# Kernel optimization log

Measured on AMD Instinct MI355X. Metric: run time of the kernel, lower is better.

## Reference

```python
import jax, jax.numpy as jnp
import numpy as np

NUM_HEADS = 8


def setup_inputs() -> dict:
    key0 = jax.random.key(0)
    ks = jax.random.split(key0, 12)
    N, M, B, C = 512, 512, 1, 256
    inp = {
        "query": jax.random.normal(ks[0], (N, B, C), dtype=jnp.float32),
        "key": jax.random.normal(ks[1], (M, B, C), dtype=jnp.float32),
        "value": jax.random.normal(ks[2], (M, B, C), dtype=jnp.float32),
        "embed_g": jax.random.normal(ks[3], (B, N, M, C), dtype=jnp.float32),
        "Wq": jax.random.normal(ks[4], (C, C), dtype=jnp.float32) * 0.02,
        "bq": jnp.zeros((C,), dtype=jnp.float32),
        "Wk": jax.random.normal(ks[5], (C, C), dtype=jnp.float32) * 0.02,
        "bk": jnp.zeros((C,), dtype=jnp.float32),
        "Wv": jax.random.normal(ks[6], (C, C), dtype=jnp.float32) * 0.02,
        "bv": jnp.zeros((C,), dtype=jnp.float32),
        "Wg": jax.random.normal(ks[7], (C, C), dtype=jnp.float32) * 0.02,
        "bg": jnp.zeros((C,), dtype=jnp.float32),
    }
    return inp


def reference(query, key, value, embed_g, Wq, bq, Wk, bk, Wv, bv, Wg, bg):
    H = NUM_HEADS
    N, B, C = query.shape
    M = key.shape[0]
    Dh = C // H

    # torch nn.Linear: x @ W.T + b
    q = (query @ Wq.T + bq).reshape(N, B, H, Dh).transpose(1, 2, 0, 3)   # (B,H,N,Dh)
    k = (key @ Wk.T + bk).reshape(M, B, H, Dh).transpose(1, 2, 0, 3)     # (B,H,M,Dh)
    v = (value @ Wv.T + bv).reshape(M, B, H, Dh).transpose(1, 2, 0, 3)   # (B,H,M,Dh)
    g = (embed_g @ Wg.T + bg).reshape(B, N, M, H, Dh).transpose(0, 3, 1, 2, 4)  # (B,H,N,M,Dh)

    scores_p = jnp.einsum('bhnc,bhnmc->bhnm', q, g)
    scores_e = jnp.einsum('bhnc,bhmc->bhnm', q, k)
    scores = (scores_e + scores_p) / jnp.sqrt(jnp.asarray(Dh, dtype=q.dtype))
    attn = jax.nn.softmax(scores, axis=-1)                               # (B,H,N,M)

    hidden = jnp.einsum('bhnm,bhmd->bhnd', attn, v)                      # (B,H,N,Dh)
    hidden = hidden.transpose(0, 2, 1, 3).reshape(B, N, C)               # (B,N,C)
    hidden = hidden.transpose(1, 0, 2)                                   # (N,B,C)
    return hidden, attn
```

## Files before the change

### kernel.cpp

```cpp
#include <hip/hip_runtime.h>


template <int CTRL, int RMASK>
__device__ __forceinline__ float dpp_add(float v) {
  int x = __builtin_amdgcn_update_dpp(0, __float_as_int(v), CTRL, RMASK, 0xf, false);
  return v + __int_as_float(x);
}

__global__ __launch_bounds__(256) void k_transpose(const float* __restrict__ Wq,
                                                   const float* __restrict__ Wk,
                                                   const float* __restrict__ Wv,
                                                   float* __restrict__ wt) {
  const float* W = (blockIdx.y == 0) ? Wq : (blockIdx.y == 1) ? Wk : Wv;
  float* O = wt + (size_t)blockIdx.y * 65536;
  __shared__ float t[64][65];
  const int tile = blockIdx.x;
  const int tr = (tile >> 2) * 64, tc = (tile & 3) * 64;
  const int c = threadIdx.x & 63, r0 = threadIdx.x >> 6;
#pragma unroll
  for (int i = 0; i < 16; ++i) {
    int r = r0 + i * 4;
    t[r][c] = W[(tr + r) * 256 + tc + c];
  }
  __syncthreads();
#pragma unroll
  for (int i = 0; i < 16; ++i) {
    int r = r0 + i * 4;
    O[(tc + r) * 256 + tr + c] = t[c][r];
  }
}

__global__ __launch_bounds__(256) void k_proj(const float* __restrict__ q_in,
                                              const float* __restrict__ k_in,
                                              const float* __restrict__ v_in,
                                              const float* __restrict__ bq,
                                              const float* __restrict__ bk,
                                              const float* __restrict__ bv,
                                              const float* __restrict__ wt,
                                              float* __restrict__ outb) {
  const int mat = blockIdx.y;
  const float* x = mat == 0 ? q_in : mat == 1 ? k_in : v_in;
  const float* b = mat == 0 ? bq : mat == 1 ? bk : bv;
  const float* WT = wt + (size_t)mat * 65536;
  float* out = outb + (size_t)mat * 131072;

  __shared__ float xl[8][256];
  const int tid = threadIdx.x;
  const int n0 = blockIdx.x * 8;
  for (int idx = tid; idx < 2048; idx += 256)
    xl[idx >> 8][idx & 255] = x[(n0 + (idx >> 8)) * 256 + (idx & 255)];
  __syncthreads();

  float acc[8] = {0.f, 0.f, 0.f, 0.f, 0.f, 0.f, 0.f, 0.f};
  for (int j = 0; j < 256; j += 4) {
    const float w0 = WT[(j + 0) * 256 + tid];
    const float w1 = WT[(j + 1) * 256 + tid];
    const float w2 = WT[(j + 2) * 256 + tid];
    const float w3 = WT[(j + 3) * 256 + tid];
#pragma unroll
    for (int r = 0; r < 8; ++r) {
      const float4 xv = *(const float4*)&xl[r][j];
      acc[r] += xv.x * w0 + xv.y * w1 + xv.z * w2 + xv.w * w3;
    }
  }
  const float bb = b[tid];
#pragma unroll
  for (int r = 0; r < 8; ++r) out[(n0 + r) * 256 + tid] = acc[r] + bb;
}

__global__ __launch_bounds__(256) void k_tfold(const float* __restrict__ qkv,
                                               const float* __restrict__ Wg,
                                               const float* __restrict__ bg,
                                               float* __restrict__ t_ws,
                                               float* __restrict__ qb_ws) {
  const int h = blockIdx.y;
  const int n0 = blockIdx.x * 64;
  const int tid = threadIdx.x;
  const float scale = 0.17677669529663687f;
  __shared__ float wg_s[32][256];
  __shared__ float qs[64][32];
  __shared__ float bgs[32];

  for (int idx = tid; idx < 8192; idx += 256)
    wg_s[idx >> 8][idx & 255] = Wg[(size_t)(h * 32 + (idx >> 8)) * 256 + (idx & 255)];
  for (int idx = tid; idx < 2048; idx += 256)
    qs[idx >> 5][idx & 31] = qkv[(size_t)(n0 + (idx >> 5)) * 256 + h * 32 + (idx & 31)];
  if (tid < 32) bgs[tid] = bg[h * 32 + tid];
  __syncthreads();

  float wr[32];
#pragma unroll
  for (int i = 0; i < 32; ++i) wr[i] = wg_s[i][tid];
  for (int nn = 0; nn < 64; ++nn) {
    float a = 0.f;
#pragma unroll
    for (int i = 0; i < 32; ++i) a = fmaf(qs[nn][i], wr[i], a);
    t_ws[(size_t)(n0 + nn) * 2048 + h * 256 + tid] = a * scale;
  }
  if (tid < 64) {
    float a = 0.f;
#pragma unroll
    for (int i = 0; i < 32; ++i) a = fmaf(qs[tid][i], bgs[i], a);
    qb_ws[(n0 + tid) * 8 + h] = a * scale;
  }
}

__global__ __launch_bounds__(512, 4) void k_main(const float* __restrict__ Eg,
                                                 const float* __restrict__ qkv,
                                                 const float* __restrict__ t_ws,
                                                 const float* __restrict__ qb_ws,
                                                 float* __restrict__ out) {
  const float* k_g = qkv + 131072;
  const float* v_g = qkv + 262144;
  const int n = blockIdx.x;
  const int tid = threadIdx.x;
  const int lane = tid & 63, w = tid >> 6;
  const int s = lane & 31, g = lane >> 5;
  const float scale = 0.17677669529663687f;
  float* attn = out + 131072;

  __shared__ float sc[4096];
  __shared__ float invd[8];
  __shared__ float pv[2][256];

  float t_r[8][8];
#pragma unroll
  for (int h = 0; h < 8; ++h) {
    const float4 a = *(const float4*)(t_ws + (size_t)n * 2048 + h * 256 + s * 8);
    const float4 b = *(const float4*)(t_ws + (size_t)n * 2048 + h * 256 + s * 8 + 4);
    t_r[h][0] = a.x; t_r[h][1] = a.y; t_r[h][2] = a.z; t_r[h][3] = a.w;
    t_r[h][4] = b.x; t_r[h][5] = b.y; t_r[h][6] = b.z; t_r[h][7] = b.w;
  }
  float q_r[8];
  {
    const float4 a = *(const float4*)(qkv + n * 256 + s * 8);
    const float4 b = *(const float4*)(qkv + n * 256 + s * 8 + 4);
    q_r[0] = a.x * scale; q_r[1] = a.y * scale; q_r[2] = a.z * scale; q_r[3] = a.w * scale;
    q_r[4] = b.x * scale; q_r[5] = b.y * scale; q_r[6] = b.z * scale; q_r[7] = b.w * scale;
  }
  float qb_r[8];
#pragma unroll
  for (int h = 0; h < 8; ++h) qb_r[h] = qb_ws[n * 8 + h];
  float msk[8];
#pragma unroll
  for (int h = 0; h < 8; ++h) msk[h] = ((s >> 2) == h) ? 1.f : 0.f;

  const float* E0 = Eg + ((size_t)n * 512 + w * 64 + g) * 256 + s * 8;
  const float* K0 = k_g + (size_t)(w * 64 + g) * 256 + s * 8;
  int m = w * 64 + g;

#pragma unroll 2
  for (int it = 0; it < 32; ++it) {
    const float4 e0 = *(const float4*)(E0);
    const float4 e1 = *(const float4*)(E0 + 4);
    const float4 k0 = *(const float4*)(K0);
    const float4 k1 = *(const float4*)(K0 + 4);
    float kacc;
    kacc = k0.x * q_r[0];             kacc = fmaf(k0.y, q_r[1], kacc);
    kacc = fmaf(k0.z, q_r[2], kacc);  kacc = fmaf(k0.w, q_r[3], kacc);
    kacc = fmaf(k1.x, q_r[4], kacc);  kacc = fmaf(k1.y, q_r[5], kacc);
    kacc = fmaf(k1.z, q_r[6], kacc);  kacc = fmaf(k1.w, q_r[7], kacc);
#pragma unroll
    for (int h = 0; h < 8; ++h) {
      float v = msk[h] * kacc;
      v = fmaf(e0.x, t_r[h][0], v); v = fmaf(e0.y, t_r[h][1], v);
      v = fmaf(e0.z, t_r[h][2], v); v = fmaf(e0.w, t_r[h][3], v);
      v = fmaf(e1.x, t_r[h][4], v); v = fmaf(e1.y, t_r[h][5], v);
      v = fmaf(e1.z, t_r[h][6], v); v = fmaf(e1.w, t_r[h][7], v);
      v = dpp_add<0xB1, 0xf>(v);
      v = dpp_add<0x4E, 0xf>(v);
      v = dpp_add<0x141, 0xf>(v);
      v = dpp_add<0x140, 0xf>(v);
      v = dpp_add<0x142, 0xa>(v);
      if (s == 16 + h) sc[h * 512 + m] = v + qb_r[h];
    }
    E0 += 512; K0 += 512; m += 2;
  }
  __syncthreads();

  {
    float vals[8];
#pragma unroll
    for (int i = 0; i < 8; ++i) vals[i] = sc[w * 512 + lane + i * 64];
    float mx = vals[0];
#pragma unroll
    for (int i = 1; i < 8; ++i) mx = fmaxf(mx, vals[i]);
#pragma unroll
    for (int off = 1; off < 64; off <<= 1) mx = fmaxf(mx, __shfl_xor(mx, off));
    float sum = 0.f;
#pragma unroll
    for (int i = 0; i < 8; ++i) {
      const float e = __expf(vals[i] - mx);
      sum += e;
      sc[w * 512 + lane + i * 64] = e;
    }
#pragma unroll
    for (int off = 1; off < 64; off <<= 1) sum += __shfl_xor(sum, off);
    if (lane == 0) invd[w] = 1.f / sum;
  }
  __syncthreads();

#pragma unroll
  for (int r = 0; r < 8; ++r) {
    const int idx = tid + r * 512;
    const int h = idx >> 9, mm = idx & 511;
    attn[(size_t)h * 262144 + n * 512 + mm] = sc[idx] * invd[h];
  }

  const int c = tid & 255, half = tid >> 8, h2 = c >> 5;
  const float* pr = sc + h2 * 512 + half * 256;
  const float* vp = v_g + (size_t)half * 65536 + c;
  float acc = 0.f;
#pragma unroll 4
  for (int m4 = 0; m4 < 64; ++m4) {
    const float4 p4 = *(const float4*)(pr + m4 * 4);
    const int mb = m4 * 4;
    acc = fmaf(p4.x, vp[(size_t)(mb + 0) * 256], acc);
    acc = fmaf(p4.y, vp[(size_t)(mb + 1) * 256], acc);
    acc = fmaf(p4.z, vp[(size_t)(mb + 2) * 256], acc);
    acc = fmaf(p4.w, vp[(size_t)(mb + 3) * 256], acc);
  }
  pv[half][c] = acc;
  __syncthreads();
  if (tid < 256) out[n * 256 + tid] = (pv[0][tid] + pv[1][tid]) * invd[tid >> 5];
}

extern "C" void kernel_launch(void* const* d_in, const int* in_sizes, int n_in,
                              void* d_out, int out_size, void* d_ws, size_t ws_size,
                              hipStream_t stream) {
  const float* query = (const float*)d_in[0];
  const float* key   = (const float*)d_in[1];
  const float* value = (const float*)d_in[2];
  const float* Eg    = (const float*)d_in[3];
  const float* Wq    = (const float*)d_in[4];
  const float* bq    = (const float*)d_in[5];
  const float* Wk    = (const float*)d_in[6];
  const float* bk    = (const float*)d_in[7];
  const float* Wv    = (const float*)d_in[8];
  const float* bv    = (const float*)d_in[9];
  const float* Wg    = (const float*)d_in[10];
  const float* bg    = (const float*)d_in[11];
  float* out = (float*)d_out;

  float* ws = (float*)d_ws;
  float* wt = ws;
  float* qkv = wt + 3 * 65536;
  float* t_ws = qkv + 3 * 131072;
  float* qb_ws = t_ws + 512 * 2048;

  k_transpose<<<dim3(16, 3), 256, 0, stream>>>(Wq, Wk, Wv, wt);
  k_proj<<<dim3(64, 3), 256, 0, stream>>>(query, key, value, bq, bk, bv, wt, qkv);
  k_tfold<<<dim3(8, 8), 256, 0, stream>>>(qkv, Wg, bg, t_ws, qb_ws);
  k_main<<<dim3(512), 512, 0, stream>>>(Eg, qkv, t_ws, qb_ws, out);
}
```

Before: 105.8 us.

## Remap k_main so each wavefront reduces one full 256-wide row per iteration

The score loop now has each 64-lane wavefront read a whole row of embed_g and K as one float4 per lane. The previous layout handled two rows per wave with two float4s per lane. This halves the per-thread t_r and q_r register arrays, which permits a higher launch-bounds occupancy target (6 blocks instead of 4), and it adds one more DPP reduction step. The PV product is reorganized so each thread accumulates four output channels over a 64-row chunk with float4 V loads, followed by an 8-way shared-memory reduction. LDS rows are padded to avoid bank conflicts, at the cost of more iterations and extra shared-memory traffic.

```diff
diff --git a/kernel.cpp b/kernel.cpp
--- a/kernel.cpp
+++ b/kernel.cpp
@@ -105,7 +105,7 @@
   }
 }
 
-__global__ __launch_bounds__(512, 4) void k_main(const float* __restrict__ Eg,
+__global__ __launch_bounds__(512, 6) void k_main(const float* __restrict__ Eg,
                                                  const float* __restrict__ qkv,
                                                  const float* __restrict__ t_ws,
                                                  const float* __restrict__ qb_ws,
@@ -115,73 +115,64 @@
   const int n = blockIdx.x;
   const int tid = threadIdx.x;
   const int lane = tid & 63, w = tid >> 6;
-  const int s = lane & 31, g = lane >> 5;
+  const int hd = lane >> 3;
   const float scale = 0.17677669529663687f;
   float* attn = out + 131072;
 
-  __shared__ float sc[4096];
+  __shared__ float sc[8 * 520];
   __shared__ float invd[8];
-  __shared__ float pv[2][256];
-
-  float t_r[8][8];
+  __shared__ float pv2[8 * 260];
+
+  float t_r[8][4];
 #pragma unroll
   for (int h = 0; h < 8; ++h) {
-    const float4 a = *(const float4*)(t_ws + (size_t)n * 2048 + h * 256 + s * 8);
-    const float4 b = *(const float4*)(t_ws + (size_t)n * 2048 + h * 256 + s * 8 + 4);
+    const float4 a = *(const float4*)(t_ws + (size_t)n * 2048 + h * 256 + lane * 4);
     t_r[h][0] = a.x; t_r[h][1] = a.y; t_r[h][2] = a.z; t_r[h][3] = a.w;
-    t_r[h][4] = b.x; t_r[h][5] = b.y; t_r[h][6] = b.z; t_r[h][7] = b.w;
-  }
-  float q_r[8];
+  }
+  float q_r[4];
   {
-    const float4 a = *(const float4*)(qkv + n * 256 + s * 8);
-    const float4 b = *(const float4*)(qkv + n * 256 + s * 8 + 4);
+    const float4 a = *(const float4*)(qkv + n * 256 + lane * 4);
     q_r[0] = a.x * scale; q_r[1] = a.y * scale; q_r[2] = a.z * scale; q_r[3] = a.w * scale;
-    q_r[4] = b.x * scale; q_r[5] = b.y * scale; q_r[6] = b.z * scale; q_r[7] = b.w * scale;
   }
   float qb_r[8];
 #pragma unroll
   for (int h = 0; h < 8; ++h) qb_r[h] = qb_ws[n * 8 + h];
-  float msk[8];
-#pragma unroll
-  for (int h = 0; h < 8; ++h) msk[h] = ((s >> 2) == h) ? 1.f : 0.f;
-
-  const float* E0 = Eg + ((size_t)n * 512 + w * 64 + g) * 256 + s * 8;
-  const float* K0 = k_g + (size_t)(w * 64 + g) * 256 + s * 8;
-  int m = w * 64 + g;
+
+  const float* E0 = Eg + ((size_t)n * 512 + w * 64) * 256 + lane * 4;
+  const float* K0 = k_g + (size_t)(w * 64) * 256 + lane * 4;
 
 #pragma unroll 2
-  for (int it = 0; it < 32; ++it) {
-    const float4 e0 = *(const float4*)(E0);
-    const float4 e1 = *(const float4*)(E0 + 4);
-    const float4 k0 = *(const float4*)(K0);
-    const float4 k1 = *(const float4*)(K0 + 4);
-    float kacc;
-    kacc = k0.x * q_r[0];             kacc = fmaf(k0.y, q_r[1], kacc);
-    kacc = fmaf(k0.z, q_r[2], kacc);  kacc = fmaf(k0.w, q_r[3], kacc);
-    kacc = fmaf(k1.x, q_r[4], kacc);  kacc = fmaf(k1.y, q_r[5], kacc);
-    kacc = fmaf(k1.z, q_r[6], kacc);  kacc = fmaf(k1.w, q_r[7], kacc);
+  for (int it = 0; it < 64; ++it) {
+    const float4 e4 = *(const float4*)E0;
+    const float4 k4 = *(const float4*)K0;
+    float kacc = k4.x * q_r[0];
+    kacc = fmaf(k4.y, q_r[1], kacc);
+    kacc = fmaf(k4.z, q_r[2], kacc);
+    kacc = fmaf(k4.w, q_r[3], kacc);
+    const int m = w * 64 + it;
 #pragma unroll
     for (int h = 0; h < 8; ++h) {
-      float v = msk[h] * kacc;
-      v = fmaf(e0.x, t_r[h][0], v); v = fmaf(e0.y, t_r[h][1], v);
-      v = fmaf(e0.z, t_r[h][2], v); v = fmaf(e0.w, t_r[h][3], v);
-      v = fmaf(e1.x, t_r[h][4], v); v = fmaf(e1.y, t_r[h][5], v);
-      v = fmaf(e1.z, t_r[h][6], v); v = fmaf(e1.w, t_r[h][7], v);
+      float v = (hd == h) ? kacc : 0.f;
+      v = fmaf(e4.x, t_r[h][0], v);
+      v = fmaf(e4.y, t_r[h][1], v);
+      v = fmaf(e4.z, t_r[h][2], v);
+      v = fmaf(e4.w, t_r[h][3], v);
       v = dpp_add<0xB1, 0xf>(v);
       v = dpp_add<0x4E, 0xf>(v);
       v = dpp_add<0x141, 0xf>(v);
       v = dpp_add<0x140, 0xf>(v);
       v = dpp_add<0x142, 0xa>(v);
-      if (s == 16 + h) sc[h * 512 + m] = v + qb_r[h];
-    }
-    E0 += 512; K0 += 512; m += 2;
+      v = dpp_add<0x143, 0xc>(v);
+      if (lane == 48 + h) sc[h * 520 + m] = v + qb_r[h];
+    }
+    E0 += 256; K0 += 256;
   }
   __syncthreads();
 
   {
     float vals[8];
 #pragma unroll
-    for (int i = 0; i < 8; ++i) vals[i] = sc[w * 512 + lane + i * 64];
+    for (int i = 0; i < 8; ++i) vals[i] = sc[w * 520 + lane + i * 64];
     float mx = vals[0];
 #pragma unroll
     for (int i = 1; i < 8; ++i) mx = fmaxf(mx, vals[i]);
@@ -192,7 +183,7 @@
     for (int i = 0; i < 8; ++i) {
       const float e = __expf(vals[i] - mx);
       sum += e;
-      sc[w * 512 + lane + i * 64] = e;
+      sc[w * 520 + lane + i * 64] = e;
     }
 #pragma unroll
     for (int off = 1; off < 64; off <<= 1) sum += __shfl_xor(sum, off);
@@ -204,25 +195,35 @@
   for (int r = 0; r < 8; ++r) {
     const int idx = tid + r * 512;
     const int h = idx >> 9, mm = idx & 511;
-    attn[(size_t)h * 262144 + n * 512 + mm] = sc[idx] * invd[h];
-  }
-
-  const int c = tid & 255, half = tid >> 8, h2 = c >> 5;
-  const float* pr = sc + h2 * 512 + half * 256;
-  const float* vp = v_g + (size_t)half * 65536 + c;
-  float acc = 0.f;
+    attn[(size_t)h * 262144 + n * 512 + mm] = sc[h * 520 + mm] * invd[h];
+  }
+
+  {
+    const int c4 = (tid & 63) * 4;
+    const int mc = tid >> 6;
+    const int hh = (tid & 63) >> 3;
+    const float* pr = sc + hh * 520 + mc * 64;
+    const float* vp = v_g + (size_t)(mc * 64) * 256 + c4;
+    float4 a4 = {0.f, 0.f, 0.f, 0.f};
 #pragma unroll 4
-  for (int m4 = 0; m4 < 64; ++m4) {
-    const float4 p4 = *(const float4*)(pr + m4 * 4);
-    const int mb = m4 * 4;
-    acc = fmaf(p4.x, vp[(size_t)(mb + 0) * 256], acc);
-    acc = fmaf(p4.y, vp[(size_t)(mb + 1) * 256], acc);
-    acc = fmaf(p4.z, vp[(size_t)(mb + 2) * 256], acc);
-    acc = fmaf(p4.w, vp[(size_t)(mb + 3) * 256], acc);
-  }
-  pv[half][c] = acc;
-  __syncthreads();
-  if (tid < 256) out[n * 256 + tid] = (pv[0][tid] + pv[1][tid]) * invd[tid >> 5];
+    for (int m = 0; m < 64; ++m) {
+      const float p = pr[m];
+      const float4 v4 = *(const float4*)vp;
+      a4.x = fmaf(p, v4.x, a4.x);
+      a4.y = fmaf(p, v4.y, a4.y);
+      a4.z = fmaf(p, v4.z, a4.z);
+      a4.w = fmaf(p, v4.w, a4.w);
+      vp += 256;
+    }
+    *(float4*)&pv2[mc * 260 + c4] = a4;
+  }
+  __syncthreads();
+  if (tid < 256) {
+    float acc = 0.f;
+#pragma unroll
+    for (int mc2 = 0; mc2 < 8; ++mc2) acc += pv2[mc2 * 260 + tid];
+    out[n * 256 + tid] = acc * invd[tid >> 5];
+  }
 }
 
 extern "C" void kernel_launch(void* const* d_in, const int* in_sizes, int n_in,
```

After: 128.9 us. +21.9%, slower.

## Drop softmax-invariant bias term, consolidate score stores, split PV over m-chunks

Applied to the files above, without the earlier changes.

The q·bg bias term is constant across m for each (n, head), so softmax cancels it. The change removes its computation, its workspace and its loads in the main kernel. Instead of eight predicated LDS stores per iteration, the score loop selects into one register and does a single store, and the loop unroll goes from 2 to 4. The score buffer rows are padded to 520 floats to reduce bank conflicts. PV now splits m into 8 chunks with float4 V loads and a shared-memory reduction, which adds a small final-sum step.

```diff
diff --git a/kernel.cpp b/kernel.cpp
--- a/kernel.cpp
+++ b/kernel.cpp
@@ -70,22 +70,18 @@
 
 __global__ __launch_bounds__(256) void k_tfold(const float* __restrict__ qkv,
                                                const float* __restrict__ Wg,
-                                               const float* __restrict__ bg,
-                                               float* __restrict__ t_ws,
-                                               float* __restrict__ qb_ws) {
+                                               float* __restrict__ t_ws) {
   const int h = blockIdx.y;
   const int n0 = blockIdx.x * 64;
   const int tid = threadIdx.x;
   const float scale = 0.17677669529663687f;
   __shared__ float wg_s[32][256];
   __shared__ float qs[64][32];
-  __shared__ float bgs[32];
 
   for (int idx = tid; idx < 8192; idx += 256)
     wg_s[idx >> 8][idx & 255] = Wg[(size_t)(h * 32 + (idx >> 8)) * 256 + (idx & 255)];
   for (int idx = tid; idx < 2048; idx += 256)
     qs[idx >> 5][idx & 31] = qkv[(size_t)(n0 + (idx >> 5)) * 256 + h * 32 + (idx & 31)];
-  if (tid < 32) bgs[tid] = bg[h * 32 + tid];
   __syncthreads();
 
   float wr[32];
@@ -97,18 +93,11 @@
     for (int i = 0; i < 32; ++i) a = fmaf(qs[nn][i], wr[i], a);
     t_ws[(size_t)(n0 + nn) * 2048 + h * 256 + tid] = a * scale;
   }
-  if (tid < 64) {
-    float a = 0.f;
-#pragma unroll
-    for (int i = 0; i < 32; ++i) a = fmaf(qs[tid][i], bgs[i], a);
-    qb_ws[(n0 + tid) * 8 + h] = a * scale;
-  }
 }
 
 __global__ __launch_bounds__(512, 4) void k_main(const float* __restrict__ Eg,
                                                  const float* __restrict__ qkv,
                                                  const float* __restrict__ t_ws,
-                                                 const float* __restrict__ qb_ws,
                                                  float* __restrict__ out) {
   const float* k_g = qkv + 131072;
   const float* v_g = qkv + 262144;
@@ -116,12 +105,13 @@
   const int tid = threadIdx.x;
   const int lane = tid & 63, w = tid >> 6;
   const int s = lane & 31, g = lane >> 5;
+  const int hd = s >> 2;
   const float scale = 0.17677669529663687f;
   float* attn = out + 131072;
 
-  __shared__ float sc[4096];
+  __shared__ float sc[8 * 520];
   __shared__ float invd[8];
-  __shared__ float pv[2][256];
+  __shared__ float pv2[8 * 260];
 
   float t_r[8][8];
 #pragma unroll
@@ -138,18 +128,11 @@
     q_r[0] = a.x * scale; q_r[1] = a.y * scale; q_r[2] = a.z * scale; q_r[3] = a.w * scale;
     q_r[4] = b.x * scale; q_r[5] = b.y * scale; q_r[6] = b.z * scale; q_r[7] = b.w * scale;
   }
-  float qb_r[8];
-#pragma unroll
-  for (int h = 0; h < 8; ++h) qb_r[h] = qb_ws[n * 8 + h];
-  float msk[8];
-#pragma unroll
-  for (int h = 0; h < 8; ++h) msk[h] = ((s >> 2) == h) ? 1.f : 0.f;
 
   const float* E0 = Eg + ((size_t)n * 512 + w * 64 + g) * 256 + s * 8;
   const float* K0 = k_g + (size_t)(w * 64 + g) * 256 + s * 8;
-  int m = w * 64 + g;
-
-#pragma unroll 2
+
+#pragma unroll 4
   for (int it = 0; it < 32; ++it) {
     const float4 e0 = *(const float4*)(E0);
     const float4 e1 = *(const float4*)(E0 + 4);
@@ -160,9 +143,11 @@
     kacc = fmaf(k0.z, q_r[2], kacc);  kacc = fmaf(k0.w, q_r[3], kacc);
     kacc = fmaf(k1.x, q_r[4], kacc);  kacc = fmaf(k1.y, q_r[5], kacc);
     kacc = fmaf(k1.z, q_r[6], kacc);  kacc = fmaf(k1.w, q_r[7], kacc);
+    const int m = w * 64 + it * 2 + g;
+    float vout = 0.f;
 #pragma unroll
     for (int h = 0; h < 8; ++h) {
-      float v = msk[h] * kacc;
+      float v = (hd == h) ? kacc : 0.f;
       v = fmaf(e0.x, t_r[h][0], v); v = fmaf(e0.y, t_r[h][1], v);
       v = fmaf(e0.z, t_r[h][2], v); v = fmaf(e0.w, t_r[h][3], v);
       v = fmaf(e1.x, t_r[h][4], v); v = fmaf(e1.y, t_r[h][5], v);
@@ -172,16 +157,17 @@
       v = dpp_add<0x141, 0xf>(v);
       v = dpp_add<0x140, 0xf>(v);
       v = dpp_add<0x142, 0xa>(v);
-      if (s == 16 + h) sc[h * 512 + m] = v + qb_r[h];
-    }
-    E0 += 512; K0 += 512; m += 2;
+      vout = (s == 16 + h) ? v : vout;
+    }
+    if ((unsigned)(s - 16) < 8u) sc[(s - 16) * 520 + m] = vout;
+    E0 += 512; K0 += 512;
   }
   __syncthreads();
 
   {
     float vals[8];
 #pragma unroll
-    for (int i = 0; i < 8; ++i) vals[i] = sc[w * 512 + lane + i * 64];
+    for (int i = 0; i < 8; ++i) vals[i] = sc[w * 520 + lane + i * 64];
     float mx = vals[0];
 #pragma unroll
     for (int i = 1; i < 8; ++i) mx = fmaxf(mx, vals[i]);
@@ -192,7 +178,7 @@
     for (int i = 0; i < 8; ++i) {
       const float e = __expf(vals[i] - mx);
       sum += e;
-      sc[w * 512 + lane + i * 64] = e;
+      sc[w * 520 + lane + i * 64] = e;
     }
 #pragma unroll
     for (int off = 1; off < 64; off <<= 1) sum += __shfl_xor(sum, off);
@@ -204,25 +190,35 @@
   for (int r = 0; r < 8; ++r) {
     const int idx = tid + r * 512;
     const int h = idx >> 9, mm = idx & 511;
-    attn[(size_t)h * 262144 + n * 512 + mm] = sc[idx] * invd[h];
-  }
-
-  const int c = tid & 255, half = tid >> 8, h2 = c >> 5;
-  const float* pr = sc + h2 * 512 + half * 256;
-  const float* vp = v_g + (size_t)half * 65536 + c;
-  float acc = 0.f;
+    attn[(size_t)h * 262144 + n * 512 + mm] = sc[h * 520 + mm] * invd[h];
+  }
+
+  {
+    const int c4 = (tid & 63) * 4;
+    const int mc = tid >> 6;
+    const int hh = (tid & 63) >> 3;
+    const float* pr = sc + hh * 520 + mc * 64;
+    const float* vp = v_g + (size_t)(mc * 64) * 256 + c4;
+    float4 a4 = {0.f, 0.f, 0.f, 0.f};
 #pragma unroll 4
-  for (int m4 = 0; m4 < 64; ++m4) {
-    const float4 p4 = *(const float4*)(pr + m4 * 4);
-    const int mb = m4 * 4;
-    acc = fmaf(p4.x, vp[(size_t)(mb + 0) * 256], acc);
-    acc = fmaf(p4.y, vp[(size_t)(mb + 1) * 256], acc);
-    acc = fmaf(p4.z, vp[(size_t)(mb + 2) * 256], acc);
-    acc = fmaf(p4.w, vp[(size_t)(mb + 3) * 256], acc);
-  }
-  pv[half][c] = acc;
-  __syncthreads();
-  if (tid < 256) out[n * 256 + tid] = (pv[0][tid] + pv[1][tid]) * invd[tid >> 5];
+    for (int m = 0; m < 64; ++m) {
+      const float p = pr[m];
+      const float4 v4 = *(const float4*)vp;
+      a4.x = fmaf(p, v4.x, a4.x);
+      a4.y = fmaf(p, v4.y, a4.y);
+      a4.z = fmaf(p, v4.z, a4.z);
+      a4.w = fmaf(p, v4.w, a4.w);
+      vp += 256;
+    }
+    *(float4*)&pv2[mc * 260 + c4] = a4;
+  }
+  __syncthreads();
+  if (tid < 256) {
+    float acc = 0.f;
+#pragma unroll
+    for (int mc2 = 0; mc2 < 8; ++mc2) acc += pv2[mc2 * 260 + tid];
+    out[n * 256 + tid] = acc * invd[tid >> 5];
+  }
 }
 
 extern "C" void kernel_launch(void* const* d_in, const int* in_sizes, int n_in,
@@ -239,17 +235,15 @@
   const float* Wv    = (const float*)d_in[8];
   const float* bv    = (const float*)d_in[9];
   const float* Wg    = (const float*)d_in[10];
-  const float* bg    = (const float*)d_in[11];
   float* out = (float*)d_out;
 
   float* ws = (float*)d_ws;
   float* wt = ws;
   float* qkv = wt + 3 * 65536;
   float* t_ws = qkv + 3 * 131072;
-  float* qb_ws = t_ws + 512 * 2048;
 
   k_transpose<<<dim3(16, 3), 256, 0, stream>>>(Wq, Wk, Wv, wt);
   k_proj<<<dim3(64, 3), 256, 0, stream>>>(query, key, value, bq, bk, bv, wt, qkv);
-  k_tfold<<<dim3(8, 8), 256, 0, stream>>>(qkv, Wg, bg, t_ws, qb_ws);
-  k_main<<<dim3(512), 512, 0, stream>>>(Eg, qkv, t_ws, qb_ws, out);
-}
+  k_tfold<<<dim3(8, 8), 256, 0, stream>>>(qkv, Wg, t_ws);
+  k_main<<<dim3(512), 512, 0, stream>>>(Eg, qkv, t_ws, out);
+}
```

Result: no change. 105.2 us (-0.5%).
